# Kernel tuning notes

Measured on AMD Instinct MI355X. Metric: run time of the kernel, lower is better.

## Reference

```python
import jax, jax.numpy as jnp
import numpy as np
from jax import lax

PRE_NMS = 3000
NMS_THR = 0.7
MAX_OUT = 1000
A_NUM = 131072
BATCH = 4


def setup_inputs() -> dict:
    key = jax.random.key(0)
    k1, k2, k3, k4 = jax.random.split(key, 4)
    # Valid 3D boxes: centers in [0,128), sizes in [2,24)
    centers = jax.random.uniform(k1, (A_NUM, 3), minval=0.0, maxval=128.0)
    sizes = jax.random.uniform(k2, (A_NUM, 3), minval=2.0, maxval=24.0)
    anchors = jnp.concatenate([centers - sizes / 2, centers + sizes / 2], axis=-1)  # (y1,x1,z1,y2,x2,z2)
    predict_scores = jax.random.normal(k3, (BATCH, A_NUM), dtype=jnp.float32)
    predict_deltas = jax.random.normal(k4, (BATCH, A_NUM, 6), dtype=jnp.float32) * 0.1
    return {"anchors": anchors.astype(jnp.float32), "predict_scores": predict_scores, "predict_deltas": predict_deltas}


def apply_regress_3d(deltas, boxes):
    # boxes [N,6]=(y1,x1,z1,y2,x2,z2); deltas [N,6]=(dy,dx,dz,dh,dw,dd)
    lo, hi = boxes[:, :3], boxes[:, 3:]
    dims = hi - lo                      # (h,w,d)
    ctr = lo + 0.5 * dims               # (cy,cx,cz)
    ctr = ctr + deltas[:, :3] * dims    # shift center by delta * size
    dims = dims * jnp.exp(deltas[:, 3:])
    return jnp.concatenate([ctr - 0.5 * dims, ctr + 0.5 * dims], axis=-1)


def pairwise_iou_3d(boxes):
    # boxes [N,6] -> iou [N,N]
    lo, hi = boxes[:, :3], boxes[:, 3:]
    inter = jnp.clip(jnp.minimum(hi[:, None, :], hi[None, :, :]) - jnp.maximum(lo[:, None, :], lo[None, :, :]), 0.0)
    inter_vol = inter.prod(-1)
    vol = jnp.clip(hi - lo, 0.0).prod(-1)
    union = vol[:, None] + vol[None, :] - inter_vol
    return inter_vol / jnp.maximum(union, 1e-8)


def nms_keep(iou, thr):
    # boxes already sorted by score desc; greedy sequential suppression
    n = iou.shape[0]
    idx = jnp.arange(n)

    def step(keep, i):
        suppressed = jnp.any((iou[i] > thr) & keep & (idx < i))
        keep = keep.at[i].set(keep[i] & ~suppressed)
        return keep, None

    keep, _ = lax.scan(step, jnp.ones(n, dtype=bool), idx)
    return keep


def reference(anchors, predict_scores, predict_deltas):
    B = predict_scores.shape[0]

    def per_sample(scores_b, deltas_b):
        order = jnp.argsort(-scores_b)[:PRE_NMS]          # descending top-k
        scores = scores_b[order]
        boxes = apply_regress_3d(deltas_b[order], anchors[order])
        iou = pairwise_iou_3d(boxes)
        keep = nms_keep(lax.stop_gradient(iou), NMS_THR)
        # pack kept boxes (in score order) into fixed MAX_OUT slots, pad invalid
        prio = jnp.where(keep, jnp.arange(PRE_NMS), PRE_NMS)
        sidx = jnp.argsort(prio)[:MAX_OUT]
        valid = prio[sidx] < PRE_NMS
        props = jnp.where(valid[:, None], boxes[sidx], 0.0)
        sc = jnp.where(valid, scores[sidx], 0.0)
        return props, sc, valid

    props, sc, valid = jax.vmap(per_sample)(predict_scores, predict_deltas)
    indices = jnp.broadcast_to(jnp.arange(B, dtype=jnp.float32)[:, None], (B, MAX_OUT))
    return (props.reshape(-1, 6), sc.reshape(-1), indices.reshape(-1), valid.reshape(-1))
```

## Files before the change

kernel.cpp:

```cpp
#include <hip/hip_runtime.h>
#include <hip/hip_bf16.h>
#include <cstdint>

typedef unsigned int u32;
typedef unsigned long long u64;

#define ANUM 131072
#define BATCH 4
#define PRE 3000
#define CAP 8192
#define NW 47
#define MROW 48
#define MAXOUT 1000
#define NBUCK 64
#define BCAP 256
#define NSUB 16
#define NSPLIT 8

#define OFF_PART   0ul
#define OFF_CAND   0ul
#define OFF_DIAG   1048576ul
#define OFF_DENSE  1179648ul
#define OFF_RANKB  1441792ul
#define OFF_INFO   2097152ul
#define OFF_ROWNZ  2098176ul
#define OFF_BCNT   2100224ul
#define OFF_SCORE  2164608ul
#define OFF_BOXES  2212608ul
#define OFF_MASKS  2500608ul
#define OFF_KEPT   7108608ul
#define ZERO_WORDS 4608

__device__ __forceinline__ u32 score_key(float f) {
  u32 u = __float_as_uint(f);
  return (u & 0x80000000u) ? ~u : (u | 0x80000000u);
}

__global__ __launch_bounds__(256) void k_h12(const float* __restrict__ scores,
                                             u32* __restrict__ part,
                                             u32* __restrict__ zr ) {
  __shared__ u32 lh[4096];
  int b = blockIdx.x >> 4, sub = blockIdx.x & (NSUB - 1);
  int tid = threadIdx.x;
  if (blockIdx.x == 0) {
#pragma unroll
    for (int i = 0; i < ZERO_WORDS / 256; ++i) zr[i * 256 + tid] = 0u;
  }
  for (int i = tid; i < 4096; i += 256) lh[i] = 0;
  __syncthreads();
  const float4* src = (const float4*)(scores + (size_t)b * ANUM) + (size_t)sub * 2048;
#pragma unroll
  for (int it = 0; it < 8; ++it) {
    float4 v = src[it * 256 + tid];
    atomicAdd(&lh[score_key(v.x) >> 20], 1u);
    atomicAdd(&lh[score_key(v.y) >> 20], 1u);
    atomicAdd(&lh[score_key(v.z) >> 20], 1u);
    atomicAdd(&lh[score_key(v.w) >> 20], 1u);
  }
  __syncthreads();
  u32* P = part + (size_t)b * 4096 * NSUB;
  for (int i = tid; i < 4096; i += 256) P[i * NSUB + sub] = lh[i];
}

__global__ void k_sel12(const u32* __restrict__ part, u32* __restrict__ info) {
  int b = blockIdx.x, tid = threadIdx.x;
  __shared__ u32 strip[256];
  const u32* P = part + (size_t)b * 4096 * NSUB;
  u32 s = 0;
  for (int j = 0; j < 16; ++j) {
    int bin = 4095 - (tid * 16 + j);
    u32 acc = 0;
#pragma unroll
    for (int sub = 0; sub < NSUB; ++sub) acc += P[bin * NSUB + sub];
    s += acc;
  }
  strip[tid] = s;
  __syncthreads();
  if (tid == 0) {
    u32 c = 0; int ts = 0; u32 cb = 0;
    for (int t = 0; t < 256; ++t) {
      if (c + strip[t] >= PRE) { ts = t; cb = c; break; }
      c += strip[t];
    }
    u32 cc = cb; int b12 = 0;
    for (int r = ts * 16; r < 4096; ++r) {
      int bin = 4095 - r;
      u32 acc = 0;
      for (int sub = 0; sub < NSUB; ++sub) acc += P[bin * NSUB + sub];
      if (cc + acc >= PRE) { b12 = bin; break; }
      cc += acc;
    }
    info[8 + b] = ((u32)b12) << 20;
  }
}

__global__ __launch_bounds__(256) void k_compact(const float4* __restrict__ scores4,
                                                 const u32* __restrict__ info,
                                                 u32* __restrict__ bcnt,
                                                 u64* __restrict__ cand) {
  int t = blockIdx.x * 256 + threadIdx.x;
  int b = t >> 15;
  int e0 = (t & 32767) * 4;
  int bucket = (blockIdx.x >> 1) & (NBUCK - 1);
  u32 T = info[8 + b];
  float4 v = scores4[t];
  float fv[4] = {v.x, v.y, v.z, v.w};
#pragma unroll
  for (int q = 0; q < 4; ++q) {
    u32 key = score_key(fv[q]);
    if (key >= T) {
      u32 pos = atomicAdd(&bcnt[(u32)((b << 6) + bucket) * 16u], 1u);
      if (pos < BCAP)
        cand[(size_t)((b << 6) + bucket) * BCAP + pos] =
            ((u64)key << 32) | (u32)(~(u32)(e0 + q));
    }
  }
}

__global__ __launch_bounds__(1024) void k_gather(const u64* __restrict__ cand,
                                                 const u32* __restrict__ bcnt,
                                                 u64* __restrict__ dense,
                                                 u32* __restrict__ rankbuf,
                                                 u32* __restrict__ info) {
  int b = blockIdx.x, tid = threadIdx.x;
  __shared__ u32 pref[NBUCK + 1];
  if (tid < NBUCK) {
    u32 c = bcnt[(u32)((b << 6) + tid) * 16u];
    if (c > BCAP) c = BCAP;
    u32 inc = c;
#pragma unroll
    for (int d = 1; d < 64; d <<= 1) {
      u32 v = __shfl_up(inc, d);
      if (tid >= d) inc += v;
    }
    pref[tid + 1] = inc;
    if (tid == 0) pref[0] = 0;
  }
  for (int i = tid; i < CAP; i += 1024) rankbuf[(size_t)b * CAP + i] = 0u;
  __syncthreads();
  u32 total = pref[NBUCK]; if (total > CAP) total = CAP;
  if (tid == 0) info[20 + b] = total;
  for (int i = tid; i < CAP; i += 1024) dense[(size_t)b * CAP + i] = 0ull;
  __syncthreads();
  for (int j = tid; j < NBUCK * BCAP; j += 1024) {
    int bk = j >> 8, sl = j & (BCAP - 1);
    u32 c = pref[bk + 1] - pref[bk];
    u32 pos = pref[bk] + (u32)sl;
    if ((u32)sl < c && pos < CAP) dense[(size_t)b * CAP + pos] = cand[(size_t)((b << 6) + bk) * BCAP + sl];
  }
}

__global__ __launch_bounds__(256) void k_rank_part(const u64* __restrict__ dense,
                                                   const u32* __restrict__ info,
                                                   u32* __restrict__ rankbuf) {
  int b = blockIdx.z;
  int tid = threadIdx.x;
  int i = blockIdx.x * 256 + tid;
  int n = (int)info[20 + b];
  if (blockIdx.x * 256 >= n) return;
  int ntile = (n + 63) >> 6;
  int tper = (ntile + NSPLIT - 1) / NSPLIT;
  int t0 = blockIdx.y * tper;
  if (t0 >= ntile) return;
  int t1 = t0 + tper; if (t1 > ntile) t1 = ntile;
  const u64* Kp = dense + (size_t)b * CAP;
  u64 mykey = Kp[i];
  int lane = tid & 63;
  int rank = 0;
  for (int t = t0; t < t1; ++t) {
    u64 kv = Kp[t * 64 + lane];
    u32 klo = (u32)kv, khi = (u32)(kv >> 32);
#pragma unroll
    for (int l = 0; l < 64; ++l) {
      u32 slo = (u32)__builtin_amdgcn_readlane((int)klo, l);
      u32 shi = (u32)__builtin_amdgcn_readlane((int)khi, l);
      u64 sk = ((u64)shi << 32) | (u64)slo;
      rank += (sk > mykey) ? 1 : 0;
    }
  }
  if (rank) atomicAdd(&rankbuf[(size_t)b * CAP + i], (u32)rank);
}

__global__ __launch_bounds__(256) void k_rankreg(const u64* __restrict__ dense,
                                                 const u32* __restrict__ rankbuf,
                                                 const u32* __restrict__ info,
                                                 const float* __restrict__ anchors,
                                                 const float* __restrict__ deltas,
                                                 float* __restrict__ scoresel,
                                                 float* __restrict__ boxes) {
  int b = blockIdx.y;
  int i = blockIdx.x * 256 + threadIdx.x;
  int n = (int)info[20 + b];
  if (i >= n) return;
  u64 mykey = dense[(size_t)b * CAP + i];
  u32 rank = rankbuf[(size_t)b * CAP + i];
  if ((u32)mykey == 0u || rank >= PRE) return;
  u32 key = (u32)(mykey >> 32);
  u32 e = ~((u32)mykey);
  u32 u = (key & 0x80000000u) ? (key ^ 0x80000000u) : ~key;
  scoresel[b * PRE + rank] = __uint_as_float(u);
  const float* an = anchors + (size_t)e * 6;
  const float* de = deltas + ((size_t)b * ANUM + e) * 6;
  float* ob = boxes + ((size_t)b * PRE + rank) * 6;
#pragma unroll
  for (int d = 0; d < 3; ++d) {
    float lo = an[d], hi = an[3 + d];
    float dims = __fsub_rn(hi, lo);
    float ctr = __fadd_rn(lo, __fmul_rn(0.5f, dims));
    ctr = __fadd_rn(ctr, __fmul_rn(de[d], dims));
    float nd = __fmul_rn(dims, expf(de[3 + d]));
    float h = __fmul_rn(0.5f, nd);
    ob[d] = __fsub_rn(ctr, h);
    ob[3 + d] = __fadd_rn(ctr, h);
  }
}

__global__ void k_mask(const float* __restrict__ boxes, u64* __restrict__ masks,
                       u64* __restrict__ diag, u64* __restrict__ rownz) {
  int jblk = blockIdx.x, iblk = blockIdx.y, b = blockIdx.z;
  if (jblk < iblk) return;
  int tid = threadIdx.x;
  __shared__ float cb[64][7];
  int j0 = jblk * 64;
  {
    int jj = j0 + tid; if (jj > PRE - 1) jj = PRE - 1;
    const float* src = boxes + ((size_t)b * PRE + jj) * 6;
#pragma unroll
    for (int d = 0; d < 6; ++d) cb[tid][d] = src[d];
    float dx = fmaxf(__fsub_rn(cb[tid][3], cb[tid][0]), 0.0f);
    float dy = fmaxf(__fsub_rn(cb[tid][4], cb[tid][1]), 0.0f);
    float dz = fmaxf(__fsub_rn(cb[tid][5], cb[tid][2]), 0.0f);
    cb[tid][6] = __fmul_rn(__fmul_rn(dx, dy), dz);
  }
  __syncthreads();
  int i = iblk * 64 + tid;
  if (i >= PRE) return;
  u64 bits = 0;
  if (j0 + 63 > i) {
    const float* rb = boxes + ((size_t)b * PRE + i) * 6;
    float l0 = rb[0], l1 = rb[1], l2 = rb[2], h0 = rb[3], h1 = rb[4], h2 = rb[5];
    float dx = fmaxf(__fsub_rn(h0, l0), 0.0f);
    float dy = fmaxf(__fsub_rn(h1, l1), 0.0f);
    float dz = fmaxf(__fsub_rn(h2, l2), 0.0f);
    float vi = __fmul_rn(__fmul_rn(dx, dy), dz);
    for (int c = 0; c < 64; ++c) {
      int j = j0 + c;
      if (j > i && j < PRE) {
        float ix = fmaxf(__fsub_rn(fminf(h0, cb[c][3]), fmaxf(l0, cb[c][0])), 0.0f);
        float iy = fmaxf(__fsub_rn(fminf(h1, cb[c][4]), fmaxf(l1, cb[c][1])), 0.0f);
        float iz = fmaxf(__fsub_rn(fminf(h2, cb[c][5]), fmaxf(l2, cb[c][2])), 0.0f);
        float iv = __fmul_rn(__fmul_rn(ix, iy), iz);
        float un = fmaxf(__fsub_rn(__fadd_rn(vi, cb[c][6]), iv), 1e-8f);
        float iou = __fdiv_rn(iv, un);
        if (iou > 0.7f) bits |= (1ull << c);
      }
    }
  }
  masks[((size_t)b * PRE + i) * MROW + jblk] = bits;
  if (iblk == jblk) diag[((size_t)b * NW + jblk) * 64 + tid] = bits;
  u64 bal = __ballot(bits != 0ull);
  if (tid == 0 && bal) atomicOr(&rownz[b * NW + iblk], bal);
}

__global__ __launch_bounds__(64) void k_scan(const u64* __restrict__ masks,
                                             const u64* __restrict__ diag,
                                             const u64* __restrict__ rownz,
                                             u32* __restrict__ kept,
                                             u32* __restrict__ info) {
  int b = blockIdx.x;
  int lane = threadIdx.x;
  const u64* Mb = masks + (size_t)b * PRE * MROW;
  const u64* Db = diag + (size_t)b * NW * 64;
  const u64* Nb = rownz + b * NW;
  int wl = lane < NW ? lane : NW - 1;
  u64 rem = 0;
  int cnt = 0;

  u64 dcur = Db[lane];
  u64 nzcur = Nb[0];

  for (int c = 0; c < NW; ++c) {
    int base = c * 64;
    int nrow = (base + 64 <= PRE) ? 64 : (PRE - base);

    u64 dn = (c + 1 < NW) ? Db[(size_t)(c + 1) * 64 + lane] : 0ull;
    u64 nzn = (c + 1 < NW) ? Nb[c + 1] : 0ull;

    u32 rlo = __shfl((u32)rem, c);
    u32 rhi = __shfl((u32)(rem >> 32), c);
    u64 pending = ~(((u64)rhi << 32) | (u64)rlo);
    if (nrow < 64) pending &= ((1ull << nrow) - 1ull);

    u64 Z = __ballot(dcur != 0ull);
    u64 chain = pending & Z;
    while (chain) {
      int k = __builtin_ctzll(chain);
      u32 rl = (u32)__builtin_amdgcn_readlane((int)(u32)dcur, k);
      u32 rh = (u32)__builtin_amdgcn_readlane((int)(u32)(dcur >> 32), k);
      u64 rw = ((u64)rh << 32) | (u64)rl;
      pending &= ~rw;
      chain &= pending;
      chain &= ~(1ull << k);
    }
    u64 keep = pending;

    u64 ltmask = (lane == 0) ? 0ull : (~0ull >> (64 - lane));
    int pos = __popcll(keep & ltmask);
    if ((keep >> lane) & 1ull) kept[b * PRE + cnt + pos] = (u32)(base + lane);
    cnt += (int)__popcll(keep);

    if (cnt >= MAXOUT) break;

    u64 nz = keep & nzcur;
    while (nz) {
      int rks[8]; int m = 0; int rr = base;
#pragma unroll
      for (int s = 0; s < 8; ++s) {
        if (nz) { rr = base + __builtin_ctzll(nz); nz &= nz - 1; ++m; }
        rks[s] = rr;
      }
      u64 v[8];
#pragma unroll
      for (int s = 0; s < 8; ++s) v[s] = Mb[(size_t)rks[s] * MROW + wl];
      u64 acc = 0;
#pragma unroll
      for (int s = 0; s < 8; ++s) acc |= (s < m) ? v[s] : 0ull;
      rem |= acc;
    }

    dcur = dn;
    nzcur = nzn;
  }
  if (lane == 0) info[16 + b] = (u32)cnt;
}

__global__ void k_out(const float* __restrict__ boxes, const float* __restrict__ scoresel,
                      const u32* __restrict__ kept, const u32* __restrict__ info,
                      float* __restrict__ out) {
  int b = blockIdx.x, tid = threadIdx.x;
  int cnt = (int)info[16 + b]; if (cnt > MAXOUT) cnt = MAXOUT;
  for (int k = tid; k < MAXOUT; k += 256) {
    float pr[6] = {0.f, 0.f, 0.f, 0.f, 0.f, 0.f};
    float s = 0.f, v = 0.f;
    if (k < cnt) {
      u32 i = kept[b * PRE + k];
      const float* bx = boxes + ((size_t)b * PRE + i) * 6;
#pragma unroll
      for (int d = 0; d < 6; ++d) pr[d] = bx[d];
      s = scoresel[b * PRE + i];
      v = 1.f;
    }
    float* pp = out + ((size_t)(b * MAXOUT + k)) * 6;
#pragma unroll
    for (int d = 0; d < 6; ++d) pp[d] = pr[d];
    out[BATCH * MAXOUT * 6 + b * MAXOUT + k] = s;
    out[BATCH * MAXOUT * 7 + b * MAXOUT + k] = (float)b;
    out[BATCH * MAXOUT * 8 + b * MAXOUT + k] = v;
  }
}

extern "C" void kernel_launch(void* const* d_in, const int* in_sizes, int n_in,
                              void* d_out, int out_size, void* d_ws, size_t ws_size,
                              hipStream_t stream) {
  const float* anchors = (const float*)d_in[0];
  const float* scores  = (const float*)d_in[1];
  const float* deltas  = (const float*)d_in[2];
  float* out = (float*)d_out;

  char* w = (char*)d_ws;
  u32* part    = (u32*)(w + OFF_PART);
  u64* cand    = (u64*)(w + OFF_CAND);
  u64* diag    = (u64*)(w + OFF_DIAG);
  u64* dense   = (u64*)(w + OFF_DENSE);
  u32* rankbuf = (u32*)(w + OFF_RANKB);
  u32* info    = (u32*)(w + OFF_INFO);
  u64* rownz   = (u64*)(w + OFF_ROWNZ);
  u32* bcnt    = (u32*)(w + OFF_BCNT);
  float* scoresel = (float*)(w + OFF_SCORE);
  float* boxes = (float*)(w + OFF_BOXES);
  u64* masks   = (u64*)(w + OFF_MASKS);
  u32* kept    = (u32*)(w + OFF_KEPT);

  k_h12<<<BATCH * NSUB, 256, 0, stream>>>(scores, part, (u32*)(w + OFF_ROWNZ));
  k_sel12<<<BATCH, 256, 0, stream>>>(part, info);
  k_compact<<<BATCH * ANUM / 4 / 256, 256, 0, stream>>>((const float4*)scores, info, bcnt, cand);
  k_gather<<<BATCH, 1024, 0, stream>>>(cand, bcnt, dense, rankbuf, info);
  k_rank_part<<<dim3(CAP / 256, NSPLIT, BATCH), 256, 0, stream>>>(dense, info, rankbuf);
  k_rankreg<<<dim3(CAP / 256, BATCH), 256, 0, stream>>>(dense, rankbuf, info, anchors, deltas,
                                                        scoresel, boxes);
  k_mask<<<dim3(NW, NW, BATCH), 64, 0, stream>>>(boxes, masks, diag, rownz);
  k_scan<<<BATCH, 64, 0, stream>>>(masks, diag, rownz, kept, info);
  k_out<<<BATCH, 256, 0, stream>>>(boxes, scoresel, kept, info, out);
}
```

Baseline: 98.26 us.

## Fuse gather, box regression and output packing into preceding kernels via last-block pattern

```diff
diff --git a/kernel.cpp b/kernel.cpp
--- a/kernel.cpp
+++ b/kernel.cpp
@@ -24,6 +24,8 @@
 #define OFF_RANKB  1441792ul
 #define OFF_INFO   2097152ul
 #define OFF_ROWNZ  2098176ul
+#define OFF_DONEC  2099712ul
+#define OFF_DONER  2099728ul
 #define OFF_BCNT   2100224ul
 #define OFF_SCORE  2164608ul
 #define OFF_BOXES  2212608ul
@@ -97,8 +99,13 @@
 __global__ __launch_bounds__(256) void k_compact(const float4* __restrict__ scores4,
                                                  const u32* __restrict__ info,
                                                  u32* __restrict__ bcnt,
-                                                 u64* __restrict__ cand) {
-  int t = blockIdx.x * 256 + threadIdx.x;
+                                                 u64* __restrict__ cand,
+                                                 u64* __restrict__ dense,
+                                                 u32* __restrict__ rankbuf,
+                                                 u32* __restrict__ donec,
+                                                 u32* __restrict__ infow) {
+  int tid = threadIdx.x;
+  int t = blockIdx.x * 256 + tid;
   int b = t >> 15;
   int e0 = (t & 32767) * 4;
   int bucket = (blockIdx.x >> 1) & (NBUCK - 1);
@@ -115,14 +122,14 @@
             ((u64)key << 32) | (u32)(~(u32)(e0 + q));
     }
   }
-}
-
-__global__ __launch_bounds__(1024) void k_gather(const u64* __restrict__ cand,
-                                                 const u32* __restrict__ bcnt,
-                                                 u64* __restrict__ dense,
-                                                 u32* __restrict__ rankbuf,
-                                                 u32* __restrict__ info) {
-  int b = blockIdx.x, tid = threadIdx.x;
+  __threadfence();
+  __syncthreads();
+  __shared__ u32 isLast;
+  if (tid == 0) isLast = (atomicAdd(&donec[b], 1u) == 127u) ? 1u : 0u;
+  __syncthreads();
+  if (!isLast) return;
+  __threadfence();
+
   __shared__ u32 pref[NBUCK + 1];
   if (tid < NBUCK) {
     u32 c = bcnt[(u32)((b << 6) + tid) * 16u];
@@ -130,88 +137,96 @@
     u32 inc = c;
 #pragma unroll
     for (int d = 1; d < 64; d <<= 1) {
-      u32 v = __shfl_up(inc, d);
-      if (tid >= d) inc += v;
+      u32 vv = __shfl_up(inc, d);
+      if (tid >= d) inc += vv;
     }
     pref[tid + 1] = inc;
     if (tid == 0) pref[0] = 0;
   }
-  for (int i = tid; i < CAP; i += 1024) rankbuf[(size_t)b * CAP + i] = 0u;
   __syncthreads();
   u32 total = pref[NBUCK]; if (total > CAP) total = CAP;
-  if (tid == 0) info[20 + b] = total;
-  for (int i = tid; i < CAP; i += 1024) dense[(size_t)b * CAP + i] = 0ull;
-  __syncthreads();
-  for (int j = tid; j < NBUCK * BCAP; j += 1024) {
+  if (tid == 0) infow[20 + b] = total;
+  for (int i = tid; i < CAP; i += 256) {
+    rankbuf[(size_t)b * CAP + i] = 0u;
+    dense[(size_t)b * CAP + i] = 0ull;
+  }
+  __syncthreads();
+  for (int j = tid; j < NBUCK * BCAP; j += 256) {
     int bk = j >> 8, sl = j & (BCAP - 1);
     u32 c = pref[bk + 1] - pref[bk];
     u32 pos = pref[bk] + (u32)sl;
-    if ((u32)sl < c && pos < CAP) dense[(size_t)b * CAP + pos] = cand[(size_t)((b << 6) + bk) * BCAP + sl];
+    if ((u32)sl < c && pos < CAP)
+      dense[(size_t)b * CAP + pos] = cand[(size_t)((b << 6) + bk) * BCAP + sl];
   }
 }
 
 __global__ __launch_bounds__(256) void k_rank_part(const u64* __restrict__ dense,
                                                    const u32* __restrict__ info,
-                                                   u32* __restrict__ rankbuf) {
+                                                   u32* __restrict__ rankbuf,
+                                                   u32* __restrict__ doner,
+                                                   const float* __restrict__ anchors,
+                                                   const float* __restrict__ deltas,
+                                                   float* __restrict__ scoresel,
+                                                   float* __restrict__ boxes) {
   int b = blockIdx.z;
   int tid = threadIdx.x;
   int i = blockIdx.x * 256 + tid;
   int n = (int)info[20 + b];
-  if (blockIdx.x * 256 >= n) return;
-  int ntile = (n + 63) >> 6;
-  int tper = (ntile + NSPLIT - 1) / NSPLIT;
-  int t0 = blockIdx.y * tper;
-  if (t0 >= ntile) return;
-  int t1 = t0 + tper; if (t1 > ntile) t1 = ntile;
   const u64* Kp = dense + (size_t)b * CAP;
-  u64 mykey = Kp[i];
-  int lane = tid & 63;
-  int rank = 0;
-  for (int t = t0; t < t1; ++t) {
-    u64 kv = Kp[t * 64 + lane];
-    u32 klo = (u32)kv, khi = (u32)(kv >> 32);
-#pragma unroll
-    for (int l = 0; l < 64; ++l) {
-      u32 slo = (u32)__builtin_amdgcn_readlane((int)klo, l);
-      u32 shi = (u32)__builtin_amdgcn_readlane((int)khi, l);
-      u64 sk = ((u64)shi << 32) | (u64)slo;
-      rank += (sk > mykey) ? 1 : 0;
-    }
-  }
-  if (rank) atomicAdd(&rankbuf[(size_t)b * CAP + i], (u32)rank);
-}
-
-__global__ __launch_bounds__(256) void k_rankreg(const u64* __restrict__ dense,
-                                                 const u32* __restrict__ rankbuf,
-                                                 const u32* __restrict__ info,
-                                                 const float* __restrict__ anchors,
-                                                 const float* __restrict__ deltas,
-                                                 float* __restrict__ scoresel,
-                                                 float* __restrict__ boxes) {
-  int b = blockIdx.y;
-  int i = blockIdx.x * 256 + threadIdx.x;
-  int n = (int)info[20 + b];
-  if (i >= n) return;
-  u64 mykey = dense[(size_t)b * CAP + i];
-  u32 rank = rankbuf[(size_t)b * CAP + i];
-  if ((u32)mykey == 0u || rank >= PRE) return;
-  u32 key = (u32)(mykey >> 32);
-  u32 e = ~((u32)mykey);
-  u32 u = (key & 0x80000000u) ? (key ^ 0x80000000u) : ~key;
-  scoresel[b * PRE + rank] = __uint_as_float(u);
-  const float* an = anchors + (size_t)e * 6;
-  const float* de = deltas + ((size_t)b * ANUM + e) * 6;
-  float* ob = boxes + ((size_t)b * PRE + rank) * 6;
-#pragma unroll
-  for (int d = 0; d < 3; ++d) {
-    float lo = an[d], hi = an[3 + d];
-    float dims = __fsub_rn(hi, lo);
-    float ctr = __fadd_rn(lo, __fmul_rn(0.5f, dims));
-    ctr = __fadd_rn(ctr, __fmul_rn(de[d], dims));
-    float nd = __fmul_rn(dims, expf(de[3 + d]));
-    float h = __fmul_rn(0.5f, nd);
-    ob[d] = __fsub_rn(ctr, h);
-    ob[3 + d] = __fadd_rn(ctr, h);
+
+  if (blockIdx.x * 256 < n) {
+    int ntile = (n + 63) >> 6;
+    int tper = (ntile + NSPLIT - 1) / NSPLIT;
+    int t0 = blockIdx.y * tper;
+    if (t0 < ntile) {
+      int t1 = t0 + tper; if (t1 > ntile) t1 = ntile;
+      u64 mykey = Kp[i];
+      int lane = tid & 63;
+      int rank = 0;
+      for (int t = t0; t < t1; ++t) {
+        u64 kv = Kp[t * 64 + lane];
+        u32 klo = (u32)kv, khi = (u32)(kv >> 32);
+#pragma unroll
+        for (int l = 0; l < 64; ++l) {
+          u32 slo = (u32)__builtin_amdgcn_readlane((int)klo, l);
+          u32 shi = (u32)__builtin_amdgcn_readlane((int)khi, l);
+          u64 sk = ((u64)shi << 32) | (u64)slo;
+          rank += (sk > mykey) ? 1 : 0;
+        }
+      }
+      if (rank) atomicAdd(&rankbuf[(size_t)b * CAP + i], (u32)rank);
+    }
+  }
+  __threadfence();
+  __syncthreads();
+  __shared__ u32 isLast;
+  if (tid == 0) isLast = (atomicAdd(&doner[b], 1u) == 255u) ? 1u : 0u;
+  __syncthreads();
+  if (!isLast) return;
+  __threadfence();
+
+  for (int k = tid; k < n; k += 256) {
+    u64 mykey = Kp[k];
+    u32 rank = rankbuf[(size_t)b * CAP + k];
+    if ((u32)mykey == 0u || rank >= PRE) continue;
+    u32 key = (u32)(mykey >> 32);
+    u32 e = ~((u32)mykey);
+    u32 u = (key & 0x80000000u) ? (key ^ 0x80000000u) : ~key;
+    scoresel[b * PRE + rank] = __uint_as_float(u);
+    const float* an = anchors + (size_t)e * 6;
+    const float* de = deltas + ((size_t)b * ANUM + e) * 6;
+    float* ob = boxes + ((size_t)b * PRE + rank) * 6;
+#pragma unroll
+    for (int d = 0; d < 3; ++d) {
+      float lo = an[d], hi = an[3 + d];
+      float dims = __fsub_rn(hi, lo);
+      float ctr = __fadd_rn(lo, __fmul_rn(0.5f, dims));
+      ctr = __fadd_rn(ctr, __fmul_rn(de[d], dims));
+      float nd = __fmul_rn(dims, expf(de[3 + d]));
+      float h = __fmul_rn(0.5f, nd);
+      ob[d] = __fsub_rn(ctr, h);
+      ob[3 + d] = __fadd_rn(ctr, h);
+    }
   }
 }
 
@@ -266,7 +281,10 @@
                                              const u64* __restrict__ diag,
                                              const u64* __restrict__ rownz,
                                              u32* __restrict__ kept,
-                                             u32* __restrict__ info) {
+                                             u32* __restrict__ info,
+                                             const float* __restrict__ boxes,
+                                             const float* __restrict__ scoresel,
+                                             float* __restrict__ out) {
   int b = blockIdx.x;
   int lane = threadIdx.x;
   const u64* Mb = masks + (size_t)b * PRE * MROW;
@@ -332,30 +350,26 @@
     nzcur = nzn;
   }
   if (lane == 0) info[16 + b] = (u32)cnt;
-}
-
-__global__ void k_out(const float* __restrict__ boxes, const float* __restrict__ scoresel,
-                      const u32* __restrict__ kept, const u32* __restrict__ info,
-                      float* __restrict__ out) {
-  int b = blockIdx.x, tid = threadIdx.x;
-  int cnt = (int)info[16 + b]; if (cnt > MAXOUT) cnt = MAXOUT;
-  for (int k = tid; k < MAXOUT; k += 256) {
+  __syncthreads();
+
+  int cc = cnt > MAXOUT ? MAXOUT : cnt;
+  for (int k = lane; k < MAXOUT; k += 64) {
     float pr[6] = {0.f, 0.f, 0.f, 0.f, 0.f, 0.f};
-    float s = 0.f, v = 0.f;
-    if (k < cnt) {
+    float s = 0.f, vfl = 0.f;
+    if (k < cc) {
       u32 i = kept[b * PRE + k];
       const float* bx = boxes + ((size_t)b * PRE + i) * 6;
 #pragma unroll
       for (int d = 0; d < 6; ++d) pr[d] = bx[d];
       s = scoresel[b * PRE + i];
-      v = 1.f;
+      vfl = 1.f;
     }
     float* pp = out + ((size_t)(b * MAXOUT + k)) * 6;
 #pragma unroll
     for (int d = 0; d < 6; ++d) pp[d] = pr[d];
     out[BATCH * MAXOUT * 6 + b * MAXOUT + k] = s;
     out[BATCH * MAXOUT * 7 + b * MAXOUT + k] = (float)b;
-    out[BATCH * MAXOUT * 8 + b * MAXOUT + k] = v;
+    out[BATCH * MAXOUT * 8 + b * MAXOUT + k] = vfl;
   }
 }
 
@@ -375,6 +389,8 @@
   u32* rankbuf = (u32*)(w + OFF_RANKB);
   u32* info    = (u32*)(w + OFF_INFO);
   u64* rownz   = (u64*)(w + OFF_ROWNZ);
+  u32* donec   = (u32*)(w + OFF_DONEC);
+  u32* doner   = (u32*)(w + OFF_DONER);
   u32* bcnt    = (u32*)(w + OFF_BCNT);
   float* scoresel = (float*)(w + OFF_SCORE);
   float* boxes = (float*)(w + OFF_BOXES);
@@ -383,12 +399,11 @@
 
   k_h12<<<BATCH * NSUB, 256, 0, stream>>>(scores, part, (u32*)(w + OFF_ROWNZ));
   k_sel12<<<BATCH, 256, 0, stream>>>(part, info);
-  k_compact<<<BATCH * ANUM / 4 / 256, 256, 0, stream>>>((const float4*)scores, info, bcnt, cand);
-  k_gather<<<BATCH, 1024, 0, stream>>>(cand, bcnt, dense, rankbuf, info);
-  k_rank_part<<<dim3(CAP / 256, NSPLIT, BATCH), 256, 0, stream>>>(dense, info, rankbuf);
-  k_rankreg<<<dim3(CAP / 256, BATCH), 256, 0, stream>>>(dense, rankbuf, info, anchors, deltas,
-                                                        scoresel, boxes);
+  k_compact<<<BATCH * ANUM / 4 / 256, 256, 0, stream>>>((const float4*)scores, info, bcnt,
+                                                        cand, dense, rankbuf, donec, info);
+  k_rank_part<<<dim3(CAP / 256, NSPLIT, BATCH), 256, 0, stream>>>(dense, info, rankbuf, doner,
+                                                                  anchors, deltas, scoresel,
+                                                                  boxes);
   k_mask<<<dim3(NW, NW, BATCH), 64, 0, stream>>>(boxes, masks, diag, rownz);
-  k_scan<<<BATCH, 64, 0, stream>>>(masks, diag, rownz, kept, info);
-  k_out<<<BATCH, 256, 0, stream>>>(boxes, scoresel, kept, info, out);
-}
+  k_scan<<<BATCH, 64, 0, stream>>>(masks, diag, rownz, kept, info, boxes, scoresel, out);
+}
```

After: 227.5 us. +131.5%, slower.
